# Kernel tuning notes

Measured on AMD Instinct MI355X. Metric: run time of the kernel, lower is better.

Reference implementation:

```python
import jax, jax.numpy as jnp
import numpy as np

HEADS = 16
DIM_HEAD = 64
SCALE = DIM_HEAD ** -0.5


def setup_inputs() -> dict:
    key = jax.random.key(0)
    k1, k2, k3 = jax.random.split(key, 3)
    B, N, D = 4, 4096, 1024
    inner = HEADS * DIM_HEAD  # 1024
    x = jax.random.normal(k1, (B, N, D), dtype=jnp.float32)
    w_qkv = jax.random.normal(k2, (D, 3 * inner), dtype=jnp.float32) * (D ** -0.5)
    w_out = jax.random.normal(k3, (inner, D), dtype=jnp.float32) * (inner ** -0.5)
    b_out = jnp.zeros((D,), dtype=jnp.float32)
    return {"x": x, "w_qkv": w_qkv, "w_out": w_out, "b_out": b_out}


def reference(x, w_qkv, w_out, b_out):
    B, N, D = x.shape
    inner = HEADS * DIM_HEAD
    qkv = x @ w_qkv  # [B, N, 3*inner]
    q, k, v = jnp.split(qkv, 3, axis=-1)

    def to_heads(t):  # [B, N, inner] -> [B, H, N, Dh]
        return t.reshape(B, N, HEADS, DIM_HEAD).transpose(0, 2, 1, 3)

    q, k, v = to_heads(q), to_heads(k), to_heads(v)
    q = jax.nn.softmax(q * SCALE, axis=-1)   # softmax over feature dim d
    k = jax.nn.softmax(k, axis=-2)           # softmax over sequence dim n
    # context[d, e] = sum_n q[n, d] * k[n, e]
    context = jnp.einsum('bhnd,bhne->bhde', q, k)
    # out[n, e] = sum_d context[d, e] * v[n, d]
    out = jnp.einsum('bhde,bhnd->bhne', context, v)
    out = out.transpose(0, 2, 1, 3).reshape(B, N, inner)  # [B, N, inner]
    return out @ w_out + b_out
```

## Files before the change

### kernel.cpp

```cpp
#include <hip/hip_runtime.h>
#include <hip/hip_bf16.h>

#define SEQ    4096
#define SCALE  0.125f

typedef __attribute__((ext_vector_type(8))) short s8v;
typedef __attribute__((ext_vector_type(8))) unsigned short u8v;
typedef __attribute__((ext_vector_type(4))) float f4v;

__device__ __forceinline__ unsigned short f2bf(float f){
  unsigned int u = __builtin_bit_cast(unsigned int, f);
  u += 0x7FFFu + ((u >> 16) & 1u);
  return (unsigned short)(u >> 16);
}

typedef const __attribute__((address_space(1))) unsigned int gl_uint;
typedef __attribute__((address_space(3))) unsigned int lds_uint;

__device__ __forceinline__ void gload_lds16(const unsigned short* g, unsigned short* l){
  __builtin_amdgcn_global_load_lds((gl_uint*)g, (lds_uint*)l, 16, 0, 0);
}

#define MM(a,b,c) __builtin_amdgcn_mfma_f32_16x16x32_bf16(a,b,c,0,0,0)
#define BAR() __builtin_amdgcn_s_barrier()
#define SB0() __builtin_amdgcn_sched_barrier(0)
#define LGKM0() do{ asm volatile("s_waitcnt lgkmcnt(0)" ::: "memory"); SB0(); }while(0)
#define VMW(n) asm volatile("s_waitcnt vmcnt(" #n ")" ::: "memory")

__device__ __forceinline__ void mfmaH0(const s8v (&A)[8], const s8v (&B)[4], f4v (&acc)[8][4]){
#pragma unroll
  for (int m = 0; m < 4; m++)
#pragma unroll
    for (int n = 0; n < 4; n++) acc[m][n] = MM(A[m], B[n], acc[m][n]);
}
__device__ __forceinline__ void mfmaH1(const s8v (&A)[8], const s8v (&B)[4], f4v (&acc)[8][4]){
#pragma unroll
  for (int m = 4; m < 8; m++)
#pragma unroll
    for (int n = 0; n < 4; n++) acc[m][n] = MM(A[m], B[n], acc[m][n]);
}

__device__ __forceinline__ void mainloop_ab(
    const unsigned short* __restrict__ Ag,
    const unsigned short* __restrict__ Bg,
    int bm, int bn, f4v (&acc)[8][4])
{
  __shared__ __align__(16) unsigned short lds[32768];
  const int tid  = threadIdx.x;
  const int wave = tid >> 6, lane = tid & 63;
  const int quad = lane >> 4, l16 = lane & 15;
  const int wmi  = wave >> 2, wni = wave & 3;
  const char* ldsc = (const char*)lds;

  const int c16   = (quad ^ ((l16 >> 1) & 3)) * 16;
  const int abase = (wmi * 128 + l16) * 64 + c16;
  const int bbase = 16384 + (wni * 64 + l16) * 64 + c16;

  const int schunk = (((tid & 3) ^ ((tid >> 3) & 3)) * 8);
  const unsigned short* aS = Ag + (size_t)(bm + (tid >> 2)) * 1024 + schunk;
  const unsigned short* bS = Bg + (size_t)(bn + (tid >> 2)) * 1024 + schunk;
  unsigned short* ldsw = lds + wave * 512;

#define STG_A(t_) do{ unsigned short* d_ = ldsw + ((t_) & 1) * 16384; \
    const unsigned short* s_ = aS + (t_) * 32; \
    gload_lds16(s_, d_); gload_lds16(s_ + 128 * 1024, d_ + 4096); }while(0)
#define STG_B(t_) do{ unsigned short* d_ = ldsw + ((t_) & 1) * 16384 + 8192; \
    const unsigned short* s_ = bS + (t_) * 32; \
    gload_lds16(s_, d_); gload_lds16(s_ + 128 * 1024, d_ + 4096); }while(0)

#define LD_B4(NB, base_) do{ \
    NB[0] = *(const s8v*)((base_) + bbase);        NB[1] = *(const s8v*)((base_) + bbase + 1024); \
    NB[2] = *(const s8v*)((base_) + bbase + 2048); NB[3] = *(const s8v*)((base_) + bbase + 3072); }while(0)
#define LD_A4LO(NA, base_) do{ \
    NA[0] = *(const s8v*)((base_) + abase);        NA[1] = *(const s8v*)((base_) + abase + 1024); \
    NA[2] = *(const s8v*)((base_) + abase + 2048); NA[3] = *(const s8v*)((base_) + abase + 3072); }while(0)
#define LD_A4HI(NA, base_) do{ \
    NA[4] = *(const s8v*)((base_) + abase + 4096); NA[5] = *(const s8v*)((base_) + abase + 5120); \
    NA[6] = *(const s8v*)((base_) + abase + 6144); NA[7] = *(const s8v*)((base_) + abase + 7168); }while(0)

  s8v A0[8], B0[4], A1[8], B1[4];

  STG_A(0); STG_B(0); STG_A(1); STG_B(1);
  VMW(4); BAR();
  LD_B4(B0, ldsc); LD_A4LO(A0, ldsc); LD_A4HI(A0, ldsc);

#define BODY(T_, CA, CB, NA, NB, DOSTG) do{ \
    LGKM0(); VMW(0); BAR(); SB0(); \
    if (DOSTG){ STG_A((T_) + 2); STG_B((T_) + 2); } \
    { const char* nb_ = ldsc + ((((T_) + 1) & 1) << 15); \
      LD_B4(NB, nb_); LD_A4LO(NA, nb_); \
      __builtin_amdgcn_s_setprio(1); mfmaH0(CA, CB, acc); __builtin_amdgcn_s_setprio(0); \
      LD_A4HI(NA, nb_); \
      __builtin_amdgcn_s_setprio(1); mfmaH1(CA, CB, acc); __builtin_amdgcn_s_setprio(0); } \
  }while(0)

  for (int t = 0; t < 30; t += 2){
    BODY(t,     A0, B0, A1, B1, 1);
    BODY(t + 1, A1, B1, A0, B0, (t + 1) <= 29);
  }
  BODY(30, A0, B0, A1, B1, 0);
  __builtin_amdgcn_s_setprio(1);
  mfmaH0(A1, B1, acc); mfmaH1(A1, B1, acc);
  __builtin_amdgcn_s_setprio(0);

#undef BODY
#undef LD_B4
#undef LD_A4LO
#undef LD_A4HI
#undef STG_A
#undef STG_B
}

__device__ __forceinline__ void mainloop_apk(
    const unsigned short* __restrict__ Ag,
    const unsigned short* __restrict__ Bpk,
    int bm, int bn, f4v (&acc)[8][4])
{
  __shared__ __align__(16) unsigned short lds[32768];
  const int tid  = threadIdx.x;
  const int wave = tid >> 6, lane = tid & 63;
  const int quad = lane >> 4, l16 = lane & 15;
  const int wmi  = wave >> 2, wni = wave & 3;
  const char* ldsc = (const char*)lds;

  const int c16   = (quad ^ ((l16 >> 1) & 3)) * 16;
  const int abase = (wmi * 128 + l16) * 64 + c16;

  const int schunk = (((tid & 3) ^ ((tid >> 3) & 3)) * 8);
  const unsigned short* aS = Ag + (size_t)(bm + (tid >> 2)) * 1024 + schunk;
  unsigned short* ldsw = lds + wave * 512;

  const unsigned short* bP = Bpk + ((size_t)((bn >> 4) + wni * 4) * 2048 + lane) * 8;

#define STG_A2(t_) do{ unsigned short* d_ = ldsw + ((t_) & 3) * 8192; \
    const unsigned short* s_ = aS + (t_) * 32; \
    gload_lds16(s_, d_); gload_lds16(s_ + 128 * 1024, d_ + 4096); }while(0)

#define LDB2(t_, BN) do{ \
    BN[0] = *(const s8v*)(bP +         (t_) * 512); \
    BN[1] = *(const s8v*)(bP + 16384 + (t_) * 512); \
    BN[2] = *(const s8v*)(bP + 32768 + (t_) * 512); \
    BN[3] = *(const s8v*)(bP + 49152 + (t_) * 512); }while(0)

#define LD2_A4LO(NA, base_) do{ const char* p_ = (base_); \
    NA[0] = *(const s8v*)(p_ + abase);        NA[1] = *(const s8v*)(p_ + abase + 1024); \
    NA[2] = *(const s8v*)(p_ + abase + 2048); NA[3] = *(const s8v*)(p_ + abase + 3072); }while(0)
#define LD2_A4HI(NA, base_) do{ const char* p_ = (base_); \
    NA[4] = *(const s8v*)(p_ + abase + 4096); NA[5] = *(const s8v*)(p_ + abase + 5120); \
    NA[6] = *(const s8v*)(p_ + abase + 6144); NA[7] = *(const s8v*)(p_ + abase + 7168); }while(0)

  s8v A0[8], B0[4], A1[8], B1[4];

  STG_A2(0); STG_A2(1); STG_A2(2);
  LDB2(0, B0);
  VMW(8); BAR();
  LD2_A4LO(A0, ldsc); LD2_A4HI(A0, ldsc);

#define BODY2(T_, CA, CB, NA, NB, DOSTG, DOLD) do{ \
    SB0(); VMW(6); BAR(); SB0(); \
    if (DOSTG) STG_A2((T_) + 3); \
    if (DOLD)  LDB2((T_) + 1, NB); \
    if (DOLD)  LD2_A4LO(NA, ldsc + ((((T_) + 1) & 3) << 14)); \
    __builtin_amdgcn_s_setprio(1); mfmaH0(CA, CB, acc); __builtin_amdgcn_s_setprio(0); \
    if (DOLD)  LD2_A4HI(NA, ldsc + ((((T_) + 1) & 3) << 14)); \
    __builtin_amdgcn_s_setprio(1); mfmaH1(CA, CB, acc); __builtin_amdgcn_s_setprio(0); \
  }while(0)

  for (int t = 0; t < 28; t += 2){
    BODY2(t,     A0, B0, A1, B1, 1, 1);
    BODY2(t + 1, A1, B1, A0, B0, 1, 1);
  }
  BODY2(28, A0, B0, A1, B1, 1, 1);
  BODY2(29, A1, B1, A0, B0, 0, 1);
  BODY2(30, A0, B0, A1, B1, 0, 1);
  BODY2(31, A1, B1, A0, B0, 0, 0);

#undef BODY2
#undef LD2_A4LO
#undef LD2_A4HI
#undef LDB2
#undef STG_A2
}

__global__ __launch_bounds__(512, 2) void qkv_gemm(
    const unsigned short* __restrict__ A,
    const unsigned short* __restrict__ Bt,
    unsigned short* __restrict__ qt,
    unsigned short* __restrict__ kt,
    unsigned short* __restrict__ vb)
{
  const int id  = blockIdx.x;
  const int swz = (id & 7) * 96 + (id >> 3);
  const int bm  = (swz / 12) * 256, bn = (swz % 12) * 256;

  f4v acc[8][4];
#pragma unroll
  for (int i = 0; i < 8; i++)
#pragma unroll
    for (int j = 0; j < 4; j++) acc[i][j] = (f4v){0.f,0.f,0.f,0.f};

  mainloop_ab(A, Bt, bm, bn, acc);

  const int tid = threadIdx.x;
  const int wave = tid >> 6, lane = tid & 63;
  const int quad = lane >> 4, l16 = lane & 15;
  const int wmi = wave >> 2, wni = wave & 3;
  const int colbase = bn + wni * 64;
  const int rowbase = bm + wmi * 128;
  const int sec = colbase >> 10;

  if (sec == 2){
#pragma unroll
    for (int nf = 0; nf < 4; nf++){
      int vc = colbase + nf * 16 + l16 - 2048;
#pragma unroll
      for (int mf = 0; mf < 8; mf++){
        int row = rowbase + mf * 16 + quad * 4;
#pragma unroll
        for (int r = 0; r < 4; r++)
          vb[(size_t)(row + r) * 1024 + vc] = f2bf(acc[mf][nf][r]);
      }
    }
    return;
  }

  if (sec == 0){
#pragma unroll
    for (int mf = 0; mf < 8; mf++){
#pragma unroll
      for (int r = 0; r < 4; r++){
        float m = fmaxf(fmaxf(acc[mf][0][r], acc[mf][1][r]),
                        fmaxf(acc[mf][2][r], acc[mf][3][r]));
        for (int off = 8; off; off >>= 1) m = fmaxf(m, __shfl_xor(m, off));
        m *= SCALE;
        float e0 = __expf(acc[mf][0][r] * SCALE - m);
        float e1 = __expf(acc[mf][1][r] * SCALE - m);
        float e2 = __expf(acc[mf][2][r] * SCALE - m);
        float e3 = __expf(acc[mf][3][r] * SCALE - m);
        float s = (e0 + e1) + (e2 + e3);
        for (int off = 8; off; off >>= 1) s += __shfl_xor(s, off);
        float inv = 1.f / s;
        acc[mf][0][r] = e0 * inv; acc[mf][1][r] = e1 * inv;
        acc[mf][2][r] = e2 * inv; acc[mf][3][r] = e3 * inv;
      }
    }
#pragma unroll
    for (int nf = 0; nf < 4; nf++){
      int col = colbase + nf * 16 + l16;
      int h = (col >> 6) & 15, de = col & 63;
#pragma unroll
      for (int mf = 0; mf < 8; mf++){
        int row = rowbase + mf * 16 + quad * 4;
        int bb = row >> 12, nl = row & 4095;
        ushort4 o;
        o.x = f2bf(acc[mf][nf][0]); o.y = f2bf(acc[mf][nf][1]);
        o.z = f2bf(acc[mf][nf][2]); o.w = f2bf(acc[mf][nf][3]);
        *(ushort4*)&qt[(((size_t)bb * 16 + h) * 64 + de) * SEQ + nl] = o;
      }
    }
  } else {
#pragma unroll
    for (int nf = 0; nf < 4; nf++){
      int col = colbase + nf * 16 + l16;
      int h = (col >> 6) & 15, de = col & 63;
#pragma unroll
      for (int mf = 0; mf < 8; mf++){
        int row = rowbase + mf * 16 + quad * 4;
        int bb = row >> 12, nl = row & 4095;
        ushort4 o;
        o.x = f2bf(__expf(acc[mf][nf][0])); o.y = f2bf(__expf(acc[mf][nf][1]));
        o.z = f2bf(__expf(acc[mf][nf][2])); o.w = f2bf(__expf(acc[mf][nf][3]));
        *(ushort4*)&kt[(((size_t)bb * 16 + h) * 64 + de) * SEQ + nl] = o;
      }
    }
  }
}

__global__ __launch_bounds__(512, 2) void gemm_final(
    const unsigned short* __restrict__ A,
    const unsigned short* __restrict__ C2pk,
    float* __restrict__ Cf,
    const float* __restrict__ bias)
{
  const int id  = blockIdx.x;
  const int swz = (id & 7) * 32 + (id >> 3);
  const int bm  = (swz >> 2) * 256, bn = (swz & 3) * 256;
  const unsigned short* Bpk = C2pk + (size_t)(bm >> 12) * 1024 * 1024;

  f4v acc[8][4];
#pragma unroll
  for (int i = 0; i < 8; i++)
#pragma unroll
    for (int j = 0; j < 4; j++) acc[i][j] = (f4v){0.f,0.f,0.f,0.f};

  mainloop_apk(A, Bpk, bm, bn, acc);

  const int tid = threadIdx.x;
  const int wave = tid >> 6, lane = tid & 63;
  const int quad = lane >> 4, l16 = lane & 15;
  const int wmi = wave >> 2, wni = wave & 3;

#pragma unroll
  for (int nf = 0; nf < 4; nf++){
    int col = bn + wni * 64 + nf * 16 + l16;
    float bv = bias[col];
#pragma unroll
    for (int mf = 0; mf < 8; mf++){
      int row = bm + wmi * 128 + mf * 16 + quad * 4;
#pragma unroll
      for (int r = 0; r < 4; r++)
        Cf[(size_t)(row + r) * 1024 + col] = acc[mf][nf][r] + bv;
    }
  }
}

__global__ void cvt_f32_bf16(const float4* __restrict__ in, ushort4* __restrict__ outp){
  int i = blockIdx.x * 256 + threadIdx.x;
  float4 v = in[i];
  ushort4 o;
  o.x = f2bf(v.x); o.y = f2bf(v.y); o.z = f2bf(v.z); o.w = f2bf(v.w);
  outp[i] = o;
}

__global__ __launch_bounds__(256) void transpose_cvt(const float* __restrict__ in,
                                                     unsigned short* __restrict__ outp,
                                                     int R, int C){
  __shared__ float tile[64][65];
  int r0 = blockIdx.y * 64, c0 = blockIdx.x * 64;
  int t = threadIdx.x;
  for (int i = t; i < 4096; i += 256){ int r = i >> 6, c = i & 63;
    tile[r][c] = in[(size_t)(r0 + r) * C + c0 + c]; }
  __syncthreads();
  for (int i = t; i < 4096; i += 256){ int c = i >> 6, r = i & 63;
    outp[(size_t)(c0 + c) * R + r0 + r] = f2bf(tile[r][c]); }
}

__global__ __launch_bounds__(256) void ctx_partial(const unsigned short* __restrict__ qt,
                                                   const unsigned short* __restrict__ kt,
                                                   float* __restrict__ ctxp){
  __shared__ float red[4096];
  int bh = blockIdx.x >> 2, ch = blockIdx.x & 3;
  int t = threadIdx.x, wave = t >> 6, lane = t & 63, quad = lane >> 4, l16 = lane & 15;
  const unsigned short* qb = qt + (size_t)bh * 64 * SEQ;
  const unsigned short* kb = kt + (size_t)bh * 64 * SEQ;
  f4v acc[4][4];
#pragma unroll
  for (int i = 0; i < 4; i++)
#pragma unroll
    for (int j = 0; j < 4; j++) acc[i][j] = (f4v){0.f,0.f,0.f,0.f};
  int ns = ch * 1024 + wave * 256;
  for (int n0 = ns; n0 < ns + 256; n0 += 32){
    s8v af[4], bf[4];
#pragma unroll
    for (int mt = 0; mt < 4; mt++) af[mt] = *(const s8v*)&qb[(size_t)(mt*16 + l16) * SEQ + n0 + quad*8];
#pragma unroll
    for (int nt = 0; nt < 4; nt++) bf[nt] = *(const s8v*)&kb[(size_t)(nt*16 + l16) * SEQ + n0 + quad*8];
#pragma unroll
    for (int mt = 0; mt < 4; mt++)
#pragma unroll
      for (int nt = 0; nt < 4; nt++)
        acc[mt][nt] = __builtin_amdgcn_mfma_f32_16x16x32_bf16(af[mt], bf[nt], acc[mt][nt], 0, 0, 0);
  }
  for (int i = t; i < 4096; i += 256) red[i] = 0.f;
  __syncthreads();
  for (int w = 0; w < 4; w++){
    if (wave == w){
#pragma unroll
      for (int mt = 0; mt < 4; mt++)
#pragma unroll
        for (int nt = 0; nt < 4; nt++)
#pragma unroll
          for (int r = 0; r < 4; r++)
            red[(mt*16 + quad*4 + r) * 64 + nt*16 + l16] += acc[mt][nt][r];
    }
    __syncthreads();
  }
  float* cp = ctxp + (size_t)blockIdx.x * 4096;
  for (int i = t; i < 4096; i += 256) cp[i] = red[i];
}

__global__ __launch_bounds__(256) void ctx2_kernel(const float* __restrict__ ctxp,
                                                   const float* __restrict__ w_out,
                                                   unsigned short* __restrict__ ctx2t){
  __shared__ float ctxs[4096];
  __shared__ float inv_s[64];
  int bh = blockIdx.x >> 4, fc = blockIdx.x & 15;
  int b = bh >> 4, h = bh & 15;
  int t = threadIdx.x;
  int fl = t & 63, dg = t >> 6;
  int f = fc * 64 + fl;
  for (int i = t; i < 4096; i += 256){
    const float* p = ctxp + (size_t)bh * 4 * 4096 + i;
    ctxs[i] = (p[0] + p[4096]) + (p[8192] + p[12288]);
  }
  __syncthreads();
  if (t < 64){
    float s = 0.f;
#pragma unroll
    for (int d = 0; d < 64; d++) s += ctxs[d * 64 + t];
    inv_s[t] = 1.f / s;
  }
  __syncthreads();
  float acc[16];
#pragma unroll
  for (int i = 0; i < 16; i++) acc[i] = 0.f;
  for (int e = 0; e < 64; e++){
    float w = w_out[(size_t)(h * 64 + e) * 1024 + f] * inv_s[e];
#pragma unroll
    for (int dd = 0; dd < 16; dd++)
      acc[dd] += ctxs[(dg * 16 + dd) * 64 + e] * w;
  }
  unsigned short* base = ctx2t + (size_t)b * 1024 * 1024;
#pragma unroll
  for (int g = 0; g < 4; g++){
    int k = h * 64 + dg * 16 + g * 4;
    int kt = k >> 5, quad = (k >> 3) & 3, e0 = k & 7;
    size_t idx = ((size_t)(f >> 4) * 2048 + (size_t)kt * 64 + quad * 16 + (f & 15)) * 8 + e0;
    ushort4 o;
    o.x = f2bf(acc[g*4+0]); o.y = f2bf(acc[g*4+1]);
    o.z = f2bf(acc[g*4+2]); o.w = f2bf(acc[g*4+3]);
    *(ushort4*)&base[idx] = o;
  }
}

extern "C" void kernel_launch(void* const* d_in, const int* in_sizes, int n_in,
                              void* d_out, int out_size, void* d_ws, size_t ws_size,
                              hipStream_t stream) {
  const float* x     = (const float*)d_in[0];
  const float* w_qkv = (const float*)d_in[1];
  const float* w_out = (const float*)d_in[2];
  const float* b_out = (const float*)d_in[3];
  float* out = (float*)d_out;

  const int M = 4 * SEQ;

  unsigned short* xb = (unsigned short*)d_out;

  char* wp = (char*)d_ws;
  size_t off = 0;
  auto nxt = [&](size_t bytes) -> char* {
    char* p = wp + off;
    off += (bytes + 255) & ~(size_t)255;
    return p;
  };
  unsigned short* wqkvT = (unsigned short*)nxt((size_t)3072 * 1024 * 2);
  unsigned short* qt    = (unsigned short*)nxt((size_t)64 * 64 * SEQ * 2);
  unsigned short* kt    = (unsigned short*)nxt((size_t)64 * 64 * SEQ * 2);
  unsigned short* vb    = (unsigned short*)nxt((size_t)M * 1024 * 2);
  float*          ctxp  = (float*)wqkvT;
  unsigned short* ctx2t = qt;

  cvt_f32_bf16<<<(M * 1024) / 4 / 256, 256, 0, stream>>>((const float4*)x, (ushort4*)xb);
  transpose_cvt<<<dim3(3072 / 64, 1024 / 64), 256, 0, stream>>>(w_qkv, wqkvT, 1024, 3072);

  qkv_gemm<<<768, 512, 0, stream>>>(xb, wqkvT, qt, kt, vb);

  ctx_partial<<<64 * 4, 256, 0, stream>>>(qt, kt, ctxp);

  ctx2_kernel<<<64 * 16, 256, 0, stream>>>(ctxp, w_out, ctx2t);

  gemm_final<<<256, 512, 0, stream>>>(vb, ctx2t, out, b_out);
}
```

Measured before the change: 342.1 us.

## Restructure QKV GEMM mainloop into 8-wave phased schedule with quad-buffered LDS

```diff
diff --git a/kernel.cpp b/kernel.cpp
--- a/kernel.cpp
+++ b/kernel.cpp
@@ -27,6 +27,13 @@
 #define LGKM0() do{ asm volatile("s_waitcnt lgkmcnt(0)" ::: "memory"); SB0(); }while(0)
 #define VMW(n) asm volatile("s_waitcnt vmcnt(" #n ")" ::: "memory")
 
+__device__ __forceinline__ void mfma16q(const s8v (&A)[4], const s8v (&B)[4], f4v (*acc)[4]){
+#pragma unroll
+  for (int m = 0; m < 4; m++)
+#pragma unroll
+    for (int n = 0; n < 4; n++) acc[m][n] = MM(A[m], B[n], acc[m][n]);
+}
+
 __device__ __forceinline__ void mfmaH0(const s8v (&A)[8], const s8v (&B)[4], f4v (&acc)[8][4]){
 #pragma unroll
   for (int m = 0; m < 4; m++)
@@ -40,12 +47,12 @@
     for (int n = 0; n < 4; n++) acc[m][n] = MM(A[m], B[n], acc[m][n]);
 }
 
-__device__ __forceinline__ void mainloop_ab(
+__device__ __forceinline__ void mainloop_8ph(
     const unsigned short* __restrict__ Ag,
     const unsigned short* __restrict__ Bg,
     int bm, int bn, f4v (&acc)[8][4])
 {
-  __shared__ __align__(16) unsigned short lds[32768];
+  __shared__ __align__(16) unsigned short lds[65536];
   const int tid  = threadIdx.x;
   const int wave = tid >> 6, lane = tid & 63;
   const int quad = lane >> 4, l16 = lane & 15;
@@ -61,52 +68,55 @@
   const unsigned short* bS = Bg + (size_t)(bn + (tid >> 2)) * 1024 + schunk;
   unsigned short* ldsw = lds + wave * 512;
 
-#define STG_A(t_) do{ unsigned short* d_ = ldsw + ((t_) & 1) * 16384; \
+#define STG_A(t_) do{ unsigned short* d_ = ldsw + ((t_) & 3) * 16384; \
     const unsigned short* s_ = aS + (t_) * 32; \
     gload_lds16(s_, d_); gload_lds16(s_ + 128 * 1024, d_ + 4096); }while(0)
-#define STG_B(t_) do{ unsigned short* d_ = ldsw + ((t_) & 1) * 16384 + 8192; \
+#define STG_B(t_) do{ unsigned short* d_ = ldsw + ((t_) & 3) * 16384 + 8192; \
     const unsigned short* s_ = bS + (t_) * 32; \
     gload_lds16(s_, d_); gload_lds16(s_ + 128 * 1024, d_ + 4096); }while(0)
 
-#define LD_B4(NB, base_) do{ \
-    NB[0] = *(const s8v*)((base_) + bbase);        NB[1] = *(const s8v*)((base_) + bbase + 1024); \
-    NB[2] = *(const s8v*)((base_) + bbase + 2048); NB[3] = *(const s8v*)((base_) + bbase + 3072); }while(0)
-#define LD_A4LO(NA, base_) do{ \
-    NA[0] = *(const s8v*)((base_) + abase);        NA[1] = *(const s8v*)((base_) + abase + 1024); \
-    NA[2] = *(const s8v*)((base_) + abase + 2048); NA[3] = *(const s8v*)((base_) + abase + 3072); }while(0)
-#define LD_A4HI(NA, base_) do{ \
-    NA[4] = *(const s8v*)((base_) + abase + 4096); NA[5] = *(const s8v*)((base_) + abase + 5120); \
-    NA[6] = *(const s8v*)((base_) + abase + 6144); NA[7] = *(const s8v*)((base_) + abase + 7168); }while(0)
-
-  s8v A0[8], B0[4], A1[8], B1[4];
+  s8v Af[4], Bf[4];
+
+#define RD_B(S_) do{ const char* p_ = ldsc + (((S_) & 3) << 15); \
+    Bf[0] = *(const s8v*)(p_ + bbase);        Bf[1] = *(const s8v*)(p_ + bbase + 1024); \
+    Bf[2] = *(const s8v*)(p_ + bbase + 2048); Bf[3] = *(const s8v*)(p_ + bbase + 3072); }while(0)
+#define RD_A(S_, MH) do{ const char* p_ = ldsc + (((S_) & 3) << 15) + (MH) * 4096; \
+    Af[0] = *(const s8v*)(p_ + abase);        Af[1] = *(const s8v*)(p_ + abase + 1024); \
+    Af[2] = *(const s8v*)(p_ + abase + 2048); Af[3] = *(const s8v*)(p_ + abase + 3072); }while(0)
+
+#define PHA(S_, STG_) do{ \
+    if (STG_) STG_A((S_) + 2); \
+    RD_B(S_); RD_A(S_, 0); \
+    BAR(); LGKM0(); \
+    __builtin_amdgcn_s_setprio(1); mfma16q(Af, Bf, &acc[0]); __builtin_amdgcn_s_setprio(0); \
+    BAR(); }while(0)
+
+#define PHB(S_, STG_, VW_) do{ \
+    if (STG_) STG_B((S_) + 2); \
+    RD_A(S_, 1); \
+    VW_; \
+    BAR(); LGKM0(); \
+    __builtin_amdgcn_s_setprio(1); mfma16q(Af, Bf, &acc[4]); __builtin_amdgcn_s_setprio(0); \
+    BAR(); }while(0)
 
   STG_A(0); STG_B(0); STG_A(1); STG_B(1);
   VMW(4); BAR();
-  LD_B4(B0, ldsc); LD_A4LO(A0, ldsc); LD_A4HI(A0, ldsc);
-
-#define BODY(T_, CA, CB, NA, NB, DOSTG) do{ \
-    LGKM0(); VMW(0); BAR(); SB0(); \
-    if (DOSTG){ STG_A((T_) + 2); STG_B((T_) + 2); } \
-    { const char* nb_ = ldsc + ((((T_) + 1) & 1) << 15); \
-      LD_B4(NB, nb_); LD_A4LO(NA, nb_); \
-      __builtin_amdgcn_s_setprio(1); mfmaH0(CA, CB, acc); __builtin_amdgcn_s_setprio(0); \
-      LD_A4HI(NA, nb_); \
-      __builtin_amdgcn_s_setprio(1); mfmaH1(CA, CB, acc); __builtin_amdgcn_s_setprio(0); } \
-  }while(0)
-
-  for (int t = 0; t < 30; t += 2){
-    BODY(t,     A0, B0, A1, B1, 1);
-    BODY(t + 1, A1, B1, A0, B0, (t + 1) <= 29);
-  }
-  BODY(30, A0, B0, A1, B1, 0);
-  __builtin_amdgcn_s_setprio(1);
-  mfmaH0(A1, B1, acc); mfmaH1(A1, B1, acc);
-  __builtin_amdgcn_s_setprio(0);
-
-#undef BODY
-#undef LD_B4
-#undef LD_A4LO
-#undef LD_A4HI
+
+  for (int s = 0; s < 28; s += 4){
+    PHA(s,     1); PHB(s,     1, VMW(4));
+    PHA(s + 1, 1); PHB(s + 1, 1, VMW(4));
+    PHA(s + 2, 1); PHB(s + 2, 1, VMW(4));
+    PHA(s + 3, 1); PHB(s + 3, 1, VMW(4));
+  }
+  PHA(28, 1); PHB(28, 1, VMW(4));
+  PHA(29, 1); PHB(29, 1, VMW(4));
+  PHA(30, 0); PHB(30, 0, VMW(0));
+  PHA(31, 0); PHB(31, 0, (void)0);
+
+#undef PHA
+#undef PHB
+#undef RD_A
+#undef RD_B
 #undef STG_A
 #undef STG_B
 }
@@ -199,7 +209,7 @@
 #pragma unroll
     for (int j = 0; j < 4; j++) acc[i][j] = (f4v){0.f,0.f,0.f,0.f};
 
-  mainloop_ab(A, Bt, bm, bn, acc);
+  mainloop_8ph(A, Bt, bm, bn, acc);
 
   const int tid = threadIdx.x;
   const int wave = tid >> 6, lane = tid & 63;
```

Result: no change. 336.2 us (-1.7%).
